# Performance work log

Hardware: AMD Instinct MI355X
Metric: run time of the kernel (lower is better)

Reference implementation:

```python
import jax, jax.numpy as jnp
import numpy as np

N, L, D, H = 2, 2048, 1024, 16
DK = D // H  # 64


def setup_inputs() -> dict:
    key = jax.random.key(0)
    ks = jax.random.split(key, 8)
    Xq = jax.random.normal(ks[0], (N, L, D), dtype=jnp.float32)
    Xk = jax.random.normal(ks[1], (N, L, D), dtype=jnp.float32)
    Xv = jax.random.normal(ks[2], (N, L, D), dtype=jnp.float32)
    mask_2d = jax.random.randint(ks[3], (N, L, L), 0, 2, dtype=jnp.int32)
    scale = 0.02
    Wq = jax.random.normal(ks[4], (D, D), dtype=jnp.float32) * scale
    Wk = jax.random.normal(ks[5], (D, D), dtype=jnp.float32) * scale
    Wv = jax.random.normal(ks[6], (D, D), dtype=jnp.float32) * scale
    Wo = jax.random.normal(ks[7], (D, D), dtype=jnp.float32) * scale
    return {"Xq": Xq, "Xk": Xk, "Xv": Xv, "Wq": Wq, "Wk": Wk, "Wv": Wv, "Wo": Wo, "mask_2d": mask_2d}


def reference(Xq, Xk, Xv, Wq, Wk, Wv, Wo, mask_2d):
    # Projections (bias=False). Per-head slicing in the original == reshape to [N,L,H,DK].
    Q = (Xq @ Wq).reshape(N, L, H, DK)
    K = (Xk @ Wk).reshape(N, L, H, DK)
    V = (Xv @ Wv).reshape(N, L, H, DK)
    # Scaled dot-product scores: [N, H, L, L]
    scores = jnp.einsum("blhd,bmhd->bhlm", Q, K) / jnp.sqrt(jnp.asarray(DK, scores_dtype(Q)))
    # NOTE: original uses masked_fill(mask==0, 0) BEFORE softmax (zero-fill, not -inf).
    scores = jnp.where(mask_2d[:, None, :, :] == 0, jnp.zeros((), scores.dtype), scores)
    A = jax.nn.softmax(scores, axis=-1)
    O = jnp.einsum("bhlm,bmhd->blhd", A, V).reshape(N, L, D)
    return O @ Wo


def scores_dtype(Q):
    return Q.dtype
```

## Files before the change

### kernel.cpp

```cpp
#include <hip/hip_runtime.h>
#include <hip/hip_bf16.h>

#define NB 2
#define L_SEQ 2048
#define NH 16
#define DKH 64
#define DMODEL 1024
#define MROWS (NB * L_SEQ)
#define QSCALE 0.18033688f
#define DD (DMODEL * DMODEL)

typedef __attribute__((ext_vector_type(8))) short short8;
typedef __attribute__((ext_vector_type(4))) float f32x4;

static __device__ __forceinline__ unsigned short f2bf(float f) {
    unsigned u = __float_as_uint(f);
    u += 0x7fffu + ((u >> 16) & 1u);
    return (unsigned short)(u >> 16);
}

static __device__ __forceinline__ float fexp2(float x) {
#if __has_builtin(__builtin_amdgcn_exp2f)
    return __builtin_amdgcn_exp2f(x);
#else
    return __expf(x * 0.6931471806f);
#endif
}

static __device__ __forceinline__ unsigned pk_bf16(float a, float b) {
    __hip_bfloat162 h = __float22bfloat162_rn(make_float2(a, b));
    return *reinterpret_cast<unsigned*>(&h);
}

static __device__ __forceinline__ void gll16(const void* g, void* l) {
    __builtin_amdgcn_global_load_lds(
        (const __attribute__((address_space(1))) void*)g,
        (__attribute__((address_space(3))) void*)l, 16, 0, 0);
}

__global__ __launch_bounds__(256)
void prep(const float* __restrict__ Xq, const float* __restrict__ Xk,
          const float* __restrict__ Xv, const float* __restrict__ w0,
          const float* __restrict__ w1, const float* __restrict__ w2,
          const float* __restrict__ w3, const int* __restrict__ mask,
          unsigned short* __restrict__ XB, unsigned short* __restrict__ WtB,
          unsigned long long* __restrict__ MWT)
{
    __shared__ float ts[32][33];
    const int bx = blockIdx.x;
    const int t  = threadIdx.x;

    if (bx < 12288) {
        const int z = bx >> 12;
        const float* src = (z == 0) ? Xq : (z == 1) ? Xk : Xv;
        const size_t i4 = (size_t)(bx & 4095) * 256 + t;
        float4 v = ((const float4*)src)[i4];
        ushort4 o;
        o.x = f2bf(v.x); o.y = f2bf(v.y); o.z = f2bf(v.z); o.w = f2bf(v.w);
        ((ushort4*)(XB + (size_t)z * 4194304))[i4] = o;
    } else if (bx < 16384) {
        const int idx = bx - 12288;
        const int z   = idx >> 10;
        const int rem = idx & 1023;
        const float* W = (z == 0) ? w0 : (z == 1) ? w1 : (z == 2) ? w2 : w3;
        unsigned short* Wt = WtB + (size_t)z * DD;
        const int n0 = (rem & 31) * 32;
        const int k0 = (rem >> 5) * 32;
        const int r  = t >> 3;
        const int c  = (t & 7) * 4;
        float4 v = *(const float4*)&W[(size_t)(k0 + r) * DMODEL + n0 + c];
        ts[r][c + 0] = v.x; ts[r][c + 1] = v.y;
        ts[r][c + 2] = v.z; ts[r][c + 3] = v.w;
        __syncthreads();
        ushort4 o;
        o.x = f2bf(ts[c + 0][r]); o.y = f2bf(ts[c + 1][r]);
        o.z = f2bf(ts[c + 2][r]); o.w = f2bf(ts[c + 3][r]);
        *(ushort4*)&Wt[(size_t)(n0 + r) * DMODEL + k0 + c] = o;
    } else {
        const int lane = t & 63;
        const size_t wid = (size_t)(bx - 16384) * 4 + (t >> 6);
        const int mv = mask[wid * 64 + lane];
        const unsigned long long bits = __ballot(mv != 0);
        if (lane == 0) {
            const int b   = (int)(wid >> 16);
            const int rem = (int)(wid & 65535);
            const int row = rem >> 5;
            const int wd  = rem & 31;
            MWT[((size_t)b * 32 + wd) * L_SEQ + row] = bits;
        }
    }
}

__global__ __launch_bounds__(256)
void gemm_qkv(const unsigned short* __restrict__ XB,
              const unsigned short* __restrict__ WtB,
              unsigned short* __restrict__ QKV)
{
    __shared__ __align__(16) unsigned short SMEM[16384];

    const int t    = threadIdx.x;
    const int w    = t >> 6;
    const int lane = t & 63;
    const int z    = blockIdx.z;
    const int m0   = blockIdx.y * 128;
    const int n0   = blockIdx.x * 128;

    const unsigned short* A = XB  + (size_t)z * ((size_t)MROWS * DMODEL);
    const unsigned short* B = WtB + (size_t)z * DD;

    const int srow = lane >> 2;
    const int sc4  = (lane & 3) ^ (srow & 3);

    const unsigned short* ag[2];
    const unsigned short* bg[2];
    int lao[2], lbo[2];
#pragma unroll
    for (int g = 0; g < 2; ++g) {
        const int R = w * 32 + g * 16;
        ag[g] = A + (size_t)(m0 + R + srow) * DMODEL + sc4 * 8;
        bg[g] = B + (size_t)(n0 + R + srow) * DMODEL + sc4 * 8;
        lao[g] = R * 32;
        lbo[g] = R * 32;
    }

    const int ml = lane & 15;
    const int q  = lane >> 4;
    const int wm = (w >> 1) * 64;
    const int wn = (w & 1) * 64;

    const f32x4 z4 = {0.f, 0.f, 0.f, 0.f};
    f32x4 acc[4][4];
#pragma unroll
    for (int i = 0; i < 4; ++i)
#pragma unroll
        for (int j = 0; j < 4; ++j) acc[i][j] = z4;

#pragma unroll
    for (int g = 0; g < 2; ++g) {
        gll16(ag[g], &SMEM[lao[g]]);
        gll16(bg[g], &SMEM[8192 + lbo[g]]);
    }

    for (int j = 0; j < 32; ++j) {
        const int cur = j & 1;
        __syncthreads();
        if (j < 31) {
            const int kt = (j + 1) * 32;
            const int nb = (cur ^ 1) * 4096;
#pragma unroll
            for (int g = 0; g < 2; ++g) {
                gll16(ag[g] + kt, &SMEM[nb + lao[g]]);
                gll16(bg[g] + kt, &SMEM[8192 + nb + lbo[g]]);
            }
        }
        const unsigned short* As = &SMEM[cur * 4096];
        const unsigned short* Bs = &SMEM[8192 + cur * 4096];
        short8 av[4], bv[4];
#pragma unroll
        for (int mt = 0; mt < 4; ++mt)
            av[mt] = *(const short8*)
                &As[(wm + mt * 16 + ml) * 32 + ((q ^ (ml & 3)) * 8)];
#pragma unroll
        for (int nt = 0; nt < 4; ++nt)
            bv[nt] = *(const short8*)
                &Bs[(wn + nt * 16 + ml) * 32 + ((q ^ (ml & 3)) * 8)];
#pragma unroll
        for (int mt = 0; mt < 4; ++mt)
#pragma unroll
            for (int nt = 0; nt < 4; ++nt)
                acc[mt][nt] = __builtin_amdgcn_mfma_f32_16x16x32_bf16(
                    av[mt], bv[nt], acc[mt][nt], 0, 0, 0);
    }

    unsigned short* O = QKV + (size_t)z * ((size_t)MROWS * DMODEL);
    if (z == 2) {
        __syncthreads();
        unsigned short* Ts = SMEM;
#pragma unroll
        for (int mt = 0; mt < 4; ++mt) {
            const int trow0 = wm + mt * 16 + q * 4;
            const int ch    = trow0 >> 3;
#pragma unroll
            for (int nt = 0; nt < 4; ++nt) {
                const int tcol = wn + nt * 16 + ml;
                const int pc   = (ch & 8) | ((ch & 7) ^ (tcol & 7));
                ushort4 pv;
                pv.x = f2bf(acc[mt][nt][0]); pv.y = f2bf(acc[mt][nt][1]);
                pv.z = f2bf(acc[mt][nt][2]); pv.w = f2bf(acc[mt][nt][3]);
                *(ushort4*)&Ts[tcol * 128 + pc * 8 + (trow0 & 7)] = pv;
            }
        }
        __syncthreads();
        const int bb = m0 >> 11;
        const int l0 = (m0 & (L_SEQ - 1)) + (t & 15) * 8;
        const int cr = t & 15;
#pragma unroll
        for (int it = 0; it < 8; ++it) {
            const int tcol = (t >> 4) + 16 * it;
            const int pc   = (cr & 8) | ((cr & 7) ^ (tcol & 7));
            short8 vv = *(const short8*)&Ts[tcol * 128 + pc * 8];
            const int n  = n0 + tcol;
            const int hh = n >> 6;
            const int dk = n & (DKH - 1);
            *(short8*)&O[((size_t)(bb * NH + hh) * DKH + dk) * L_SEQ + l0] = vv;
        }
    } else {
        const float qs = (z == 0) ? QSCALE : 1.0f;
#pragma unroll
        for (int mt = 0; mt < 4; ++mt) {
            const int gr0 = m0 + wm + mt * 16 + q * 4;
#pragma unroll
            for (int nt = 0; nt < 4; ++nt) {
                const int col = n0 + wn + nt * 16 + ml;
                const int hh  = col >> 6;
                const int dk  = col & (DKH - 1);
#pragma unroll
                for (int r = 0; r < 4; ++r) {
                    const int row = gr0 + r;
                    const int bb  = row >> 11;
                    const int l   = row & (L_SEQ - 1);
                    O[(((size_t)(bb * NH + hh) * L_SEQ + l) << 6) + dk] =
                        f2bf(acc[mt][nt][r] * qs);
                }
            }
        }
    }
}

__global__ __launch_bounds__(256)
void gemm_out(const unsigned short* __restrict__ OB,
              const unsigned short* __restrict__ Wt,
              float* __restrict__ out)
{
    __shared__ __align__(16) unsigned short As[2][2048];
    __shared__ __align__(16) unsigned short Bs[2][4096];

    const int t    = threadIdx.x;
    const int w    = t >> 6;
    const int lane = t & 63;
    const int m0   = blockIdx.y * 64;
    const int n0   = blockIdx.x * 128;

    const int srow = lane >> 2;
    const int sc4  = (lane & 3) ^ (srow & 3);

    const unsigned short* ag =
        OB + (size_t)(m0 + w * 16 + srow) * DMODEL + sc4 * 8;
    const unsigned short* bg[2];
    int lbo[2];
#pragma unroll
    for (int g = 0; g < 2; ++g) {
        const int R = w * 32 + g * 16;
        bg[g] = Wt + (size_t)(n0 + R + srow) * DMODEL + sc4 * 8;
        lbo[g] = R * 32;
    }
    const int lao = (w * 16) * 32;

    const int ml = lane & 15;
    const int q  = lane >> 4;
    const int wm = (w >> 1) * 32;
    const int wn = (w & 1) * 64;

    const f32x4 z4 = {0.f, 0.f, 0.f, 0.f};
    f32x4 acc[2][4];
#pragma unroll
    for (int i = 0; i < 2; ++i)
#pragma unroll
        for (int j = 0; j < 4; ++j) acc[i][j] = z4;

    gll16(ag, &As[0][lao]);
#pragma unroll
    for (int g = 0; g < 2; ++g) gll16(bg[g], &Bs[0][lbo[g]]);

    for (int j = 0; j < 32; ++j) {
        const int cur = j & 1;
        __syncthreads();
        if (j < 31) {
            const int kt = (j + 1) * 32;
            gll16(ag + kt, &As[cur ^ 1][lao]);
#pragma unroll
            for (int g = 0; g < 2; ++g)
                gll16(bg[g] + kt, &Bs[cur ^ 1][lbo[g]]);
        }
        short8 av[2], bv[4];
#pragma unroll
        for (int mt = 0; mt < 2; ++mt)
            av[mt] = *(const short8*)
                &As[cur][(wm + mt * 16 + ml) * 32 + ((q ^ (ml & 3)) * 8)];
#pragma unroll
        for (int nt = 0; nt < 4; ++nt)
            bv[nt] = *(const short8*)
                &Bs[cur][(wn + nt * 16 + ml) * 32 + ((q ^ (ml & 3)) * 8)];
#pragma unroll
        for (int mt = 0; mt < 2; ++mt)
#pragma unroll
            for (int nt = 0; nt < 4; ++nt)
                acc[mt][nt] = __builtin_amdgcn_mfma_f32_16x16x32_bf16(
                    av[mt], bv[nt], acc[mt][nt], 0, 0, 0);
    }

#pragma unroll
    for (int mt = 0; mt < 2; ++mt) {
        const int gr0 = m0 + wm + mt * 16 + q * 4;
#pragma unroll
        for (int nt = 0; nt < 4; ++nt) {
            const int col = n0 + wn + nt * 16 + ml;
#pragma unroll
            for (int r = 0; r < 4; ++r)
                out[(size_t)(gr0 + r) * DMODEL + col] = acc[mt][nt][r];
        }
    }
}

__global__ __launch_bounds__(256, 4)
void attn_mfma(const unsigned short* __restrict__ Qb,
               const unsigned short* __restrict__ Kb,
               const unsigned short* __restrict__ Vtb,
               const unsigned long long* __restrict__ MWT,
               unsigned short* __restrict__ OB)
{
    __shared__ __align__(16) unsigned short Ks[2][4096];
    __shared__ __align__(16) unsigned short Vts[2][4096];
    __shared__ __align__(16) unsigned short Ps[4][1024];

    const int t    = threadIdx.x;
    const int w    = t >> 6;
    const int lane = t & 63;
    const int ml   = lane & 15;
    const int quad = lane >> 4;

    const int bid = blockIdx.x;
    const int p   = (bid >> 8) * 8 + (bid & 7);
    const int jq  = (bid >> 3) & 31;
    const int h   = p & 15;
    const int b   = p >> 4;
    const int q0  = jq * 64;

    const size_t hoff = (size_t)(b * NH + h) * L_SEQ * DKH;
    const unsigned short* Qh  = Qb  + hoff;
    const unsigned short* Kh  = Kb  + hoff;
    const unsigned short* Vth = Vtb + hoff;

    short8 qf[2];
#pragma unroll
    for (int s = 0; s < 2; ++s)
        qf[s] = *(const short8*)
            &Qh[(size_t)(q0 + w * 16 + ml) * DKH + (s * 4 + quad) * 8];

    const int srow = lane >> 3;
    const int sc   = (lane & 7) ^ srow;

    const unsigned short* kg0 = Kh + (size_t)(w * 16 + srow) * DKH + sc * 8;
    const unsigned short* kg1 = Kh + (size_t)(w * 16 + 8 + srow) * DKH + sc * 8;
    const unsigned short* vg0 = Vth + (size_t)(w * 16 + srow) * L_SEQ + sc * 8;
    const unsigned short* vg1 = Vth + (size_t)(w * 16 + 8 + srow) * L_SEQ + sc * 8;
    const int lk0 = (w * 16) * 64;
    const int lk1 = (w * 16 + 8) * 64;

    const unsigned long long* mg_w = MWT + (size_t)b * 32 * L_SEQ + q0 + w * 16;
    unsigned long long mcur = 0, mnxt = 0;
    if (lane < 16) mcur = mg_w[lane];

    f32x4 oacc[4];
    const f32x4 z4 = {0.f, 0.f, 0.f, 0.f};
#pragma unroll
    for (int dt = 0; dt < 4; ++dt) oacc[dt] = z4;
    float l_i = 0.f;

    gll16(kg0, &Ks[0][lk0]);  gll16(kg1, &Ks[0][lk1]);
    gll16(vg0, &Vts[0][lk0]); gll16(vg1, &Vts[0][lk1]);
    kg0 += 64 * DKH; kg1 += 64 * DKH; vg0 += 64; vg1 += 64;

    for (int j = 0; j < 32; ++j) {
        const int cur = j & 1;
        __syncthreads();
        if (j < 31) {
            const int nxt = cur ^ 1;
            gll16(kg0, &Ks[nxt][lk0]);  gll16(kg1, &Ks[nxt][lk1]);
            gll16(vg0, &Vts[nxt][lk0]); gll16(vg1, &Vts[nxt][lk1]);
            kg0 += 64 * DKH; kg1 += 64 * DKH; vg0 += 64; vg1 += 64;
            if (lane < 16) mnxt = mg_w[(size_t)(j + 1) * L_SEQ + lane];
        }

        f32x4 sacc[4];
#pragma unroll
        for (int kt = 0; kt < 4; ++kt) sacc[kt] = z4;
#pragma unroll
        for (int s = 0; s < 2; ++s) {
            short8 kf[4];
#pragma unroll
            for (int kt = 0; kt < 4; ++kt)
                kf[kt] = *(const short8*)
                    &Ks[cur][(kt * 16 + ml) * 64 + (((s * 4 + quad) ^ (ml & 7)) * 8)];
#pragma unroll
            for (int kt = 0; kt < 4; ++kt)
                sacc[kt] = __builtin_amdgcn_mfma_f32_16x16x32_bf16(
                    kf[kt], qf[s], sacc[kt], 0, 0, 0);
        }

        const unsigned long long wq = __shfl(mcur, ml) >> (quad * 4);
        const unsigned mlo = (unsigned)wq;
        const unsigned mhi = (unsigned)(wq >> 32);
        float rs = 0.f;
        float pr[4][4];
#pragma unroll
        for (int kt = 0; kt < 4; ++kt) {
            const unsigned word = (kt < 2) ? mlo : mhi;
            const int base = (kt & 1) * 16;
#pragma unroll
            for (int r = 0; r < 4; ++r) {
                const float mf = (float)((word >> (base + r)) & 1u);
                const float e  = fexp2(sacc[kt][r] * mf);
                pr[kt][r] = e;
                rs += e;
            }
        }
        rs += __shfl_xor(rs, 16);
        rs += __shfl_xor(rs, 32);
        l_i += rs;
#pragma unroll
        for (int kt = 0; kt < 4; ++kt) {
            uint2 pk;
            pk.x = pk_bf16(pr[kt][0], pr[kt][1]);
            pk.y = pk_bf16(pr[kt][2], pr[kt][3]);
            const int cp = (kt * 2 + (quad >> 1)) ^ (ml & 7);
            *(uint2*)&Ps[w][ml * 64 + cp * 8 + (quad & 1) * 4] = pk;
        }

#pragma unroll
        for (int s = 0; s < 2; ++s) {
            const short8 pf = *(const short8*)
                &Ps[w][ml * 64 + (((s * 4 + quad) ^ (ml & 7)) * 8)];
#pragma unroll
            for (int dt = 0; dt < 4; ++dt) {
                const short8 vf = *(const short8*)
                    &Vts[cur][(dt * 16 + ml) * 64 + (((s * 4 + quad) ^ (ml & 7)) * 8)];
                oacc[dt] = __builtin_amdgcn_mfma_f32_16x16x32_bf16(
                    vf, pf, oacc[dt], 0, 0, 0);
            }
        }
        mcur = mnxt;
    }

    const float inv = 1.0f / l_i;
    const int qrow = q0 + w * 16 + ml;
#pragma unroll
    for (int dt = 0; dt < 4; ++dt) {
        ushort4 o4;
        o4.x = f2bf(oacc[dt][0] * inv);
        o4.y = f2bf(oacc[dt][1] * inv);
        o4.z = f2bf(oacc[dt][2] * inv);
        o4.w = f2bf(oacc[dt][3] * inv);
        *(ushort4*)&OB[(size_t)(b * L_SEQ + qrow) * DMODEL + h * DKH +
                       dt * 16 + quad * 4] = o4;
    }
}

extern "C" void kernel_launch(void* const* d_in, const int* in_sizes, int n_in,
                              void* d_out, int out_size, void* d_ws, size_t ws_size,
                              hipStream_t stream)
{
    (void)in_sizes; (void)n_in; (void)out_size; (void)ws_size;

    const float* Xq   = (const float*)d_in[0];
    const float* Xk   = (const float*)d_in[1];
    const float* Xv   = (const float*)d_in[2];
    const float* Wq   = (const float*)d_in[3];
    const float* Wk   = (const float*)d_in[4];
    const float* Wv   = (const float*)d_in[5];
    const float* Wo   = (const float*)d_in[6];
    const int*   mask = (const int*)d_in[7];
    float* out = (float*)d_out;

    char* base = (char*)d_ws;
    unsigned short*     XB  = (unsigned short*)base;
    unsigned short*     WtB = (unsigned short*)(base + (24u << 20));
    unsigned short*     QKV = (unsigned short*)(base + (32u << 20));
    unsigned short*     OB  = (unsigned short*)(base + (56u << 20));
    unsigned long long* MWT = (unsigned long long*)(base + (64u << 20));

    const size_t tsz = (size_t)MROWS * DMODEL;

    prep<<<dim3(49152), 256, 0, stream>>>(
        Xq, Xk, Xv, Wq, Wk, Wv, Wo, mask, XB, WtB, MWT);

    gemm_qkv<<<dim3(8, 32, 3), 256, 0, stream>>>(XB, WtB, QKV);

    attn_mfma<<<dim3(1024), 256, 0, stream>>>(
        QKV, QKV + tsz, QKV + 2 * tsz, MWT, OB);

    gemm_out<<<dim3(8, 64), 256, 0, stream>>>(OB, WtB + 3 * (size_t)DD, out);
}
```

Measured before the change: 273.1 us.

## Split attention key range across two wave groups with shared-memory reduction

The attention kernel now uses 512 threads, with 8 waves split into 4 query-row groups times 2 key halves. Each iteration loads a 128-key tile and each key-half group processes its own 64 keys. The partial outputs and row sums are combined through shared memory at the end. The loop is now single-buffered with two barriers per iteration instead of double-buffered with one, which trades load/compute overlap for more waves per block and fewer iterations.

```diff
diff --git a/kernel.cpp b/kernel.cpp
--- a/kernel.cpp
+++ b/kernel.cpp
@@ -312,19 +312,21 @@
     }
 }
 
-__global__ __launch_bounds__(256, 4)
+__global__ __launch_bounds__(512, 6)
 void attn_mfma(const unsigned short* __restrict__ Qb,
                const unsigned short* __restrict__ Kb,
                const unsigned short* __restrict__ Vtb,
                const unsigned long long* __restrict__ MWT,
                unsigned short* __restrict__ OB)
 {
-    __shared__ __align__(16) unsigned short Ks[2][4096];
-    __shared__ __align__(16) unsigned short Vts[2][4096];
-    __shared__ __align__(16) unsigned short Ps[4][1024];
+    __shared__ __align__(16) unsigned short Ks[128 * 64];
+    __shared__ __align__(16) unsigned short Vts[64 * 128];
+    __shared__ __align__(16) unsigned short Ps[8][512];
 
     const int t    = threadIdx.x;
     const int w    = t >> 6;
+    const int qsub = w & 3;
+    const int ksub = w >> 2;
     const int lane = t & 63;
     const int ml   = lane & 15;
     const int quad = lane >> 4;
@@ -345,21 +347,34 @@
 #pragma unroll
     for (int s = 0; s < 2; ++s)
         qf[s] = *(const short8*)
-            &Qh[(size_t)(q0 + w * 16 + ml) * DKH + (s * 4 + quad) * 8];
-
-    const int srow = lane >> 3;
-    const int sc   = (lane & 7) ^ srow;
-
-    const unsigned short* kg0 = Kh + (size_t)(w * 16 + srow) * DKH + sc * 8;
-    const unsigned short* kg1 = Kh + (size_t)(w * 16 + 8 + srow) * DKH + sc * 8;
-    const unsigned short* vg0 = Vth + (size_t)(w * 16 + srow) * L_SEQ + sc * 8;
-    const unsigned short* vg1 = Vth + (size_t)(w * 16 + 8 + srow) * L_SEQ + sc * 8;
-    const int lk0 = (w * 16) * 64;
-    const int lk1 = (w * 16 + 8) * 64;
-
-    const unsigned long long* mg_w = MWT + (size_t)b * 32 * L_SEQ + q0 + w * 16;
+            &Qh[(size_t)(q0 + qsub * 16 + ml) * DKH + (s * 4 + quad) * 8];
+
+    const int kr8 = lane >> 3;
+    const int kc  = (lane & 7) ^ kr8;
+    const unsigned short* kgp[2];
+    int lko[2];
+#pragma unroll
+    for (int g = 0; g < 2; ++g) {
+        const int R0 = w * 16 + g * 8;
+        kgp[g] = Kh + (size_t)(R0 + kr8) * DKH + kc * 8;
+        lko[g] = R0 * 64;
+    }
+    const int vr4 = lane >> 4;
+    const int vpc = lane & 15;
+    const unsigned short* vgp[2];
+    int lvo[2];
+#pragma unroll
+    for (int g = 0; g < 2; ++g) {
+        const int D0 = w * 8 + g * 4;
+        const int vc = (vpc & 8) | ((vpc & 7) ^ ((g * 4 + vr4) & 7));
+        vgp[g] = Vth + (size_t)(D0 + vr4) * L_SEQ + vc * 8;
+        lvo[g] = D0 * 128;
+    }
+
+    const unsigned long long* mg =
+        MWT + ((size_t)b * 32 + ksub) * L_SEQ + q0 + qsub * 16;
     unsigned long long mcur = 0, mnxt = 0;
-    if (lane < 16) mcur = mg_w[lane];
+    if (lane < 16) mcur = mg[lane];
 
     f32x4 oacc[4];
     const f32x4 z4 = {0.f, 0.f, 0.f, 0.f};
@@ -367,20 +382,18 @@
     for (int dt = 0; dt < 4; ++dt) oacc[dt] = z4;
     float l_i = 0.f;
 
-    gll16(kg0, &Ks[0][lk0]);  gll16(kg1, &Ks[0][lk1]);
-    gll16(vg0, &Vts[0][lk0]); gll16(vg1, &Vts[0][lk1]);
-    kg0 += 64 * DKH; kg1 += 64 * DKH; vg0 += 64; vg1 += 64;
-
-    for (int j = 0; j < 32; ++j) {
-        const int cur = j & 1;
-        __syncthreads();
-        if (j < 31) {
-            const int nxt = cur ^ 1;
-            gll16(kg0, &Ks[nxt][lk0]);  gll16(kg1, &Ks[nxt][lk1]);
-            gll16(vg0, &Vts[nxt][lk0]); gll16(vg1, &Vts[nxt][lk1]);
-            kg0 += 64 * DKH; kg1 += 64 * DKH; vg0 += 64; vg1 += 64;
-            if (lane < 16) mnxt = mg_w[(size_t)(j + 1) * L_SEQ + lane];
-        }
+    for (int j = 0; j < 16; ++j) {
+        __syncthreads();
+#pragma unroll
+        for (int g = 0; g < 2; ++g) {
+            gll16(kgp[g], &Ks[lko[g]]);
+            gll16(vgp[g], &Vts[lvo[g]]);
+            kgp[g] += 128 * DKH;
+            vgp[g] += 128;
+        }
+        if (lane < 16 && j < 15)
+            mnxt = mg[(size_t)(j + 1) * 2 * L_SEQ + lane];
+        __syncthreads();
 
         f32x4 sacc[4];
 #pragma unroll
@@ -391,7 +404,8 @@
 #pragma unroll
             for (int kt = 0; kt < 4; ++kt)
                 kf[kt] = *(const short8*)
-                    &Ks[cur][(kt * 16 + ml) * 64 + (((s * 4 + quad) ^ (ml & 7)) * 8)];
+                    &Ks[(ksub * 64 + kt * 16 + ml) * 64 +
+                        (((s * 4 + quad) ^ (ml & 7)) * 8)];
 #pragma unroll
             for (int kt = 0; kt < 4; ++kt)
                 sacc[kt] = __builtin_amdgcn_mfma_f32_16x16x32_bf16(
@@ -399,60 +413,70 @@
         }
 
         const unsigned long long wq = __shfl(mcur, ml) >> (quad * 4);
-        const unsigned mlo = (unsigned)wq;
-        const unsigned mhi = (unsigned)(wq >> 32);
         float rs = 0.f;
-        float pr[4][4];
-#pragma unroll
-        for (int kt = 0; kt < 4; ++kt) {
-            const unsigned word = (kt < 2) ? mlo : mhi;
-            const int base = (kt & 1) * 16;
-#pragma unroll
-            for (int r = 0; r < 4; ++r) {
-                const float mf = (float)((word >> (base + r)) & 1u);
-                const float e  = fexp2(sacc[kt][r] * mf);
-                pr[kt][r] = e;
-                rs += e;
+#pragma unroll
+        for (int hh2 = 0; hh2 < 2; ++hh2) {
+#pragma unroll
+            for (int ktp = 0; ktp < 2; ++ktp) {
+                const int kt = hh2 * 2 + ktp;
+                float pr[4];
+#pragma unroll
+                for (int r = 0; r < 4; ++r) {
+                    const float mf =
+                        (float)((unsigned)(wq >> (kt * 16 + r)) & 1u);
+                    pr[r] = fexp2(sacc[kt][r] * mf);
+                    rs += pr[r];
+                }
+                uint2 pk;
+                pk.x = pk_bf16(pr[0], pr[1]);
+                pk.y = pk_bf16(pr[2], pr[3]);
+                const int pc = (ktp * 2 + (quad >> 1)) ^ (ml & 3);
+                *(uint2*)&Ps[w][ml * 32 + pc * 8 + (quad & 1) * 4] = pk;
+            }
+            const short8 pf = *(const short8*)
+                &Ps[w][ml * 32 + ((quad ^ (ml & 3)) * 8)];
+#pragma unroll
+            for (int dt = 0; dt < 4; ++dt) {
+                const int vcc = ksub * 8 + hh2 * 4 + quad;
+                const int vpc2 = (vcc & 8) | ((vcc & 7) ^ (ml & 7));
+                const short8 vf = *(const short8*)
+                    &Vts[(dt * 16 + ml) * 128 + vpc2 * 8];
+                oacc[dt] = __builtin_amdgcn_mfma_f32_16x16x32_bf16(
+                    vf, pf, oacc[dt], 0, 0, 0);
             }
         }
         rs += __shfl_xor(rs, 16);
         rs += __shfl_xor(rs, 32);
         l_i += rs;
-#pragma unroll
-        for (int kt = 0; kt < 4; ++kt) {
-            uint2 pk;
-            pk.x = pk_bf16(pr[kt][0], pr[kt][1]);
-            pk.y = pk_bf16(pr[kt][2], pr[kt][3]);
-            const int cp = (kt * 2 + (quad >> 1)) ^ (ml & 7);
-            *(uint2*)&Ps[w][ml * 64 + cp * 8 + (quad & 1) * 4] = pk;
-        }
-
-#pragma unroll
-        for (int s = 0; s < 2; ++s) {
-            const short8 pf = *(const short8*)
-                &Ps[w][ml * 64 + (((s * 4 + quad) ^ (ml & 7)) * 8)];
-#pragma unroll
-            for (int dt = 0; dt < 4; ++dt) {
-                const short8 vf = *(const short8*)
-                    &Vts[cur][(dt * 16 + ml) * 64 + (((s * 4 + quad) ^ (ml & 7)) * 8)];
-                oacc[dt] = __builtin_amdgcn_mfma_f32_16x16x32_bf16(
-                    vf, pf, oacc[dt], 0, 0, 0);
-            }
-        }
         mcur = mnxt;
     }
 
-    const float inv = 1.0f / l_i;
-    const int qrow = q0 + w * 16 + ml;
-#pragma unroll
-    for (int dt = 0; dt < 4; ++dt) {
-        ushort4 o4;
-        o4.x = f2bf(oacc[dt][0] * inv);
-        o4.y = f2bf(oacc[dt][1] * inv);
-        o4.z = f2bf(oacc[dt][2] * inv);
-        o4.w = f2bf(oacc[dt][3] * inv);
-        *(ushort4*)&OB[(size_t)(b * L_SEQ + qrow) * DMODEL + h * DKH +
-                       dt * 16 + quad * 4] = o4;
+    __syncthreads();
+    float* Ored = (float*)Ks;
+    float* Lred = (float*)Ps;
+    if (ksub == 1) {
+#pragma unroll
+        for (int dt = 0; dt < 4; ++dt)
+            *(f32x4*)&Ored[(qsub * 16 + ml) * 64 + dt * 16 + quad * 4] =
+                oacc[dt];
+        if (quad == 0) Lred[qsub * 16 + ml] = l_i;
+    }
+    __syncthreads();
+    if (ksub == 0) {
+        const float inv = 1.0f / (l_i + Lred[qsub * 16 + ml]);
+        const int qrow = q0 + qsub * 16 + ml;
+#pragma unroll
+        for (int dt = 0; dt < 4; ++dt) {
+            const f32x4 oh =
+                *(const f32x4*)&Ored[(qsub * 16 + ml) * 64 + dt * 16 + quad * 4];
+            ushort4 o4;
+            o4.x = f2bf((oacc[dt][0] + oh[0]) * inv);
+            o4.y = f2bf((oacc[dt][1] + oh[1]) * inv);
+            o4.z = f2bf((oacc[dt][2] + oh[2]) * inv);
+            o4.w = f2bf((oacc[dt][3] + oh[3]) * inv);
+            *(ushort4*)&OB[(size_t)(b * L_SEQ + qrow) * DMODEL + h * DKH +
+                           dt * 16 + quad * 4] = o4;
+        }
     }
 }
 
@@ -486,7 +510,7 @@
 
     gemm_qkv<<<dim3(8, 32, 3), 256, 0, stream>>>(XB, WtB, QKV);
 
-    attn_mfma<<<dim3(1024), 256, 0, stream>>>(
+    attn_mfma<<<dim3(1024), 512, 0, stream>>>(
         QKV, QKV + tsz, QKV + 2 * tsz, MWT, OB);
 
     gemm_out<<<dim3(8, 64), 256, 0, stream>>>(OB, WtB + 3 * (size_t)DD, out);
```

Result: no change. 278.3 us (+1.9%).
